# Kernel tuning notes

Hardware: AMD Instinct MI355X
Metric: run time of the kernel (lower is better)

## Reference

```python
import jax, jax.numpy as jnp
import numpy as np

EPS = 1e-8

def rms_norm(x, scale):
    # full RMSNorm over last dim (p < 0 branch): norm/sqrt(d)
    d = x.shape[-1]
    norm = jnp.linalg.norm(x, ord=2, axis=-1, keepdims=True)
    rms = norm * (d ** -0.5)
    return scale * (x / (rms + EPS))

def setup_inputs() -> dict:
    key = jax.random.key(0)
    ks = jax.random.split(key, 4)
    B, N, C, H = 2, 2048, 1024, 16
    hd = C // H
    x = jax.random.normal(ks[0], (B, N, C), dtype=jnp.float32)
    Wqkv = jax.random.normal(ks[1], (C, 3 * C), dtype=jnp.float32) * (C ** -0.5)
    Wproj = jax.random.normal(ks[2], (C, C), dtype=jnp.float32) * (C ** -0.5)
    bproj = jnp.zeros((C,), dtype=jnp.float32)
    q_scale = jnp.ones((hd,), dtype=jnp.float32)
    k_scale = jnp.ones((hd,), dtype=jnp.float32)
    return {"x": x, "Wqkv": Wqkv, "Wproj": Wproj, "bproj": bproj,
            "q_scale": q_scale, "k_scale": k_scale}

def reference(x, Wqkv, Wproj, bproj, q_scale, k_scale):
    B, N, C = x.shape
    H = 16
    hd = C // H
    scale = hd ** -0.5
    qkv = (x @ Wqkv).reshape(B, N, 3, H, hd)
    qkv = jnp.transpose(qkv, (2, 0, 3, 1, 4))  # t b h n c
    q, k, v = qkv[0], qkv[1], qkv[2]
    q = rms_norm(q, q_scale)
    k = rms_norm(k, k_scale)
    attn = jnp.einsum('bhnc,bhmc->bhnm', q, k) * scale
    attn = jax.nn.softmax(attn, axis=-1)
    out = jnp.einsum('bhnm,bhmc->bhnc', attn, v)
    out = jnp.transpose(out, (0, 2, 1, 3)).reshape(B, N, C)
    return out @ Wproj + bproj
```

## Files before the change

### kernel.cpp

```cpp
#include <hip/hip_runtime.h>


typedef _Float16 half_t;
typedef __attribute__((ext_vector_type(2))) __fp16 fp16x2;
typedef __attribute__((ext_vector_type(4))) _Float16 half4v;
typedef __attribute__((ext_vector_type(8))) _Float16 half8;
typedef __attribute__((ext_vector_type(4))) float f32x4;

#define DI __device__ __forceinline__

DI void gl_lds16(const void* g, void* l) {
    __builtin_amdgcn_global_load_lds((const __attribute__((address_space(1))) void*)g,
                                     (__attribute__((address_space(3))) void*)l, 16, 0, 0);
}

DI float exp2_fast(float x) {
    float r;
    asm("v_exp_f32 %0, %1" : "=v"(r) : "v"(x));
    return r;
}

__global__ void prep_all(const float* __restrict__ x, const float* __restrict__ Wqkv,
                         const float* __restrict__ Wproj, half_t* __restrict__ xh,
                         half_t* __restrict__ wqt, half_t* __restrict__ wpt) {
    __shared__ float t[32][33];
    int bid = blockIdx.x;
    if (bid < 4096) {
        int i = (bid * 256 + threadIdx.x) * 4;
        float4 v = *(const float4*)(x + i);
        half4v o;
        o[0] = (half_t)v.x; o[1] = (half_t)v.y; o[2] = (half_t)v.z; o[3] = (half_t)v.w;
        *(half4v*)(xh + i) = o;
    } else if (bid < 4096 + 3072) {
        int i = bid - 4096;
        int c0 = (i % 96) * 32, r0 = (i / 96) * 32;
        int tx = threadIdx.x & 31, ty = threadIdx.x >> 5;
#pragma unroll
        for (int k = 0; k < 4; k++)
            t[ty + 8 * k][tx] = Wqkv[(size_t)(r0 + ty + 8 * k) * 3072 + c0 + tx];
        __syncthreads();
#pragma unroll
        for (int k = 0; k < 4; k++)
            wqt[(size_t)(c0 + ty + 8 * k) * 1024 + r0 + tx] = (half_t)t[tx][ty + 8 * k];
    } else {
        int i = bid - 4096 - 3072;
        int c0 = (i % 32) * 32, r0 = (i / 32) * 32;
        int tx = threadIdx.x & 31, ty = threadIdx.x >> 5;
#pragma unroll
        for (int k = 0; k < 4; k++)
            t[ty + 8 * k][tx] = Wproj[(size_t)(r0 + ty + 8 * k) * 1024 + c0 + tx];
        __syncthreads();
#pragma unroll
        for (int k = 0; k < 4; k++)
            wpt[(size_t)(c0 + ty + 8 * k) * 1024 + r0 + tx] = (half_t)t[tx][ty + 8 * k];
    }
}

__global__ __launch_bounds__(256) void gemm_qkv(
    const half_t* __restrict__ A, const half_t* __restrict__ Bt,
    const float* __restrict__ qs, const float* __restrict__ ks,
    half_t* __restrict__ qh, half_t* __restrict__ kh, half_t* __restrict__ vth) {
    const int K = 1024;
    __shared__ __align__(16) half_t Al[2][128 * 64];
    __shared__ __align__(16) half_t Bl[2][128 * 64];
    int tid = threadIdx.x;
    int w = tid >> 6, l = tid & 63;
    int wr = w >> 1, wc = w & 1;
    int g = l >> 4, r = l & 15;
    int m0 = blockIdx.x * 128, n0 = blockIdx.y * 128;
    f32x4 acc[4][4] = {};

#define STAGE_QKV(kt, buf)                                                        \
    {                                                                             \
        _Pragma("unroll")                                                         \
        for (int p = 0; p < 4; p++) {                                             \
            int ci = p * 256 + tid;                                               \
            int row = ci >> 3, c = ci & 7, lc = c ^ (row & 7);                    \
            gl_lds16(A + (size_t)(m0 + row) * K + (kt) * 64 + lc * 8,             \
                     &Al[buf][0] + ci * 8);                                       \
            gl_lds16(Bt + (size_t)(n0 + row) * K + (kt) * 64 + lc * 8,            \
                     &Bl[buf][0] + ci * 8);                                       \
        }                                                                         \
    }

    STAGE_QKV(0, 0);
    __syncthreads();
    int cur = 0;
    for (int kt = 0; kt < 16; kt++) {
        if (kt < 15) STAGE_QKV(kt + 1, cur ^ 1);
#pragma unroll
        for (int ks2 = 0; ks2 < 2; ks2++) {
            half8 af[4], bf[4];
#pragma unroll
            for (int i = 0; i < 4; i++) {
                int row = wr * 64 + i * 16 + r;
                af[i] = *(const half8*)(&Al[cur][0] + row * 64 + (((4 * ks2 + g) ^ (row & 7)) << 3));
                int rowb = wc * 64 + i * 16 + r;
                bf[i] = *(const half8*)(&Bl[cur][0] + rowb * 64 + (((4 * ks2 + g) ^ (rowb & 7)) << 3));
            }
#pragma unroll
            for (int i = 0; i < 4; i++)
#pragma unroll
                for (int j = 0; j < 4; j++)
                    acc[i][j] = __builtin_amdgcn_mfma_f32_16x16x32_f16(af[i], bf[j], acc[i][j], 0, 0, 0);
        }
        __syncthreads();
        cur ^= 1;
    }

    int tsec = n0 >> 10;
    if (tsec == 2) {
#pragma unroll
        for (int i = 0; i < 4; i++)
#pragma unroll
            for (int j = 0; j < 4; j++) {
                int gcol = n0 + wc * 64 + j * 16 + r;
                int h = (gcol >> 6) & 15;
                int f = gcol & 63;
                int growb = m0 + wr * 64 + i * 16 + g * 4;
                int b = growb >> 11;
                int n = growb & 2047;
                half4v pv;
#pragma unroll
                for (int rr = 0; rr < 4; rr++) pv[rr] = (half_t)acc[i][j][rr];
                *(half4v*)(vth + ((size_t)(b * 16 + h) * 64 + f) * 2048 + n) = pv;
            }
    } else {
        const float* sc = (tsec == 0) ? qs : ks;
        half_t* dst = (tsec == 0) ? qh : kh;
        float extra = (tsec == 0) ? (0.125f * 1.44269504f) : 1.0f;
        float scv[4];
#pragma unroll
        for (int j = 0; j < 4; j++) scv[j] = sc[j * 16 + r];
#pragma unroll
        for (int i = 0; i < 4; i++)
#pragma unroll
            for (int rr = 0; rr < 4; rr++) {
                float ss = 0.f;
#pragma unroll
                for (int j = 0; j < 4; j++) ss += acc[i][j][rr] * acc[i][j][rr];
#pragma unroll
                for (int d = 1; d < 16; d <<= 1) ss += __shfl_xor(ss, d, 64);
                float inv = extra / (sqrtf(ss) * 0.125f + 1e-8f);
                int grow = m0 + wr * 64 + i * 16 + g * 4 + rr;
                int b = grow >> 11;
                int n = grow & 2047;
#pragma unroll
                for (int j = 0; j < 4; j++) {
                    int gcol = n0 + wc * 64 + j * 16 + r;
                    int h = (gcol >> 6) & 15;
                    int f = gcol & 63;
                    dst[((size_t)(b * 16 + h) * 2048 + n) * 64 + f] =
                        (half_t)(acc[i][j][rr] * inv * scv[j]);
                }
            }
    }
}

__global__ __launch_bounds__(512, 4) void attn(
    const half_t* __restrict__ qh, const half_t* __restrict__ kh,
    const half_t* __restrict__ vth, half_t* __restrict__ aoh) {
    int bh = blockIdx.y;
    int q0 = blockIdx.x * 128;
    const half_t* Qp = qh + (size_t)bh * 2048 * 64;
    const half_t* Kp = kh + (size_t)bh * 2048 * 64;
    const half_t* Vp = vth + (size_t)bh * 64 * 2048;
    __shared__ __align__(16) half_t Kl[2][64 * 64];
    __shared__ __align__(16) half_t Vl[2][64 * 64];
    __shared__ __align__(16) half_t Pl[8][16 * 64];
    int tid = threadIdx.x, w = tid >> 6, l = tid & 63, g = l >> 4, r = l & 15;

    int srow = tid >> 3, sc = tid & 7, slc = sc ^ (srow & 7);
    const half_t* kst = Kp + (size_t)srow * 64 + slc * 8;
    const half_t* vst = Vp + (size_t)srow * 2048 + slc * 8;

    int koff[8], voff[8], poffw[4], poffr[2];
#pragma unroll
    for (int ks = 0; ks < 2; ks++)
#pragma unroll
        for (int tt = 0; tt < 4; tt++) {
            int row = tt * 16 + r;
            koff[ks * 4 + tt] = row * 64 + (((4 * ks + g) ^ (row & 7)) << 3);
        }
#pragma unroll
    for (int ks2 = 0; ks2 < 2; ks2++)
#pragma unroll
        for (int cf = 0; cf < 4; cf++) {
            int row = cf * 16 + r;
            voff[ks2 * 4 + cf] = row * 64 + (((4 * ks2 + g) ^ (row & 7)) << 3);
        }
#pragma unroll
    for (int tt = 0; tt < 4; tt++)
        poffw[tt] = r * 64 + (((2 * tt + (g >> 1)) ^ (r & 7)) << 3) + (g & 1) * 4;
#pragma unroll
    for (int ks2 = 0; ks2 < 2; ks2++)
        poffr[ks2] = r * 64 + (((4 * ks2 + g) ^ (r & 7)) << 3);
    half_t* Pw = &Pl[w][0];

    half8 qf[2];
#pragma unroll
    for (int ks = 0; ks < 2; ks++)
        qf[ks] = *(const half8*)(Qp + (size_t)(q0 + w * 16 + r) * 64 + ks * 32 + g * 8);

    f32x4 o[4] = {};
    float m = -1e30f, lsum = 0.f;

    gl_lds16(kst, &Kl[0][0] + tid * 8);
    gl_lds16(vst, &Vl[0][0] + tid * 8);
    __syncthreads();

#define ATTN_TILE(BUF, T)                                                          \
    {                                                                              \
        if ((T) < 31) {                                                            \
            gl_lds16(kst + ((T) + 1) * 4096, &Kl[(BUF) ^ 1][0] + tid * 8);         \
            gl_lds16(vst + ((T) + 1) * 64, &Vl[(BUF) ^ 1][0] + tid * 8);           \
        }                                                                          \
        const half_t* Kc = &Kl[BUF][0];                                            \
        const half_t* Vc = &Vl[BUF][0];                                            \
        f32x4 s[4] = {};                                                           \
        _Pragma("unroll")                                                          \
        for (int ks = 0; ks < 2; ks++)                                             \
            _Pragma("unroll")                                                      \
            for (int tt = 0; tt < 4; tt++) {                                       \
                half8 kf = *(const half8*)(Kc + koff[ks * 4 + tt]);                \
                s[tt] = __builtin_amdgcn_mfma_f32_16x16x32_f16(kf, qf[ks], s[tt], 0, 0, 0); \
            }                                                                      \
        float mx = -1e30f;                                                         \
        _Pragma("unroll")                                                          \
        for (int tt = 0; tt < 4; tt++)                                             \
            mx = fmaxf(mx, fmaxf(fmaxf(s[tt][0], s[tt][1]), fmaxf(s[tt][2], s[tt][3]))); \
        mx = fmaxf(mx, __shfl_xor(mx, 16, 64));                                    \
        mx = fmaxf(mx, __shfl_xor(mx, 32, 64));                                    \
        if (!__all(mx <= m + 11.0f)) {                                             \
            float mn = fmaxf(m, mx);                                               \
            float fac = exp2_fast(m - mn);                                         \
            lsum *= fac;                                                           \
            _Pragma("unroll")                                                      \
            for (int cf = 0; cf < 4; cf++) {                                       \
                o[cf][0] *= fac; o[cf][1] *= fac; o[cf][2] *= fac; o[cf][3] *= fac; \
            }                                                                      \
            m = mn;                                                                \
        }                                                                          \
        _Pragma("unroll")                                                          \
        for (int tt = 0; tt < 4; tt++)                                             \
            _Pragma("unroll")                                                      \
            for (int e = 0; e < 4; e++) {                                          \
                float p = exp2_fast(s[tt][e] - m);                                 \
                s[tt][e] = p;                                                      \
                lsum += p;                                                         \
            }                                                                      \
        _Pragma("unroll")                                                          \
        for (int tt = 0; tt < 4; tt++) {                                           \
            fp16x2 a = __builtin_amdgcn_cvt_pkrtz(s[tt][0], s[tt][1]);             \
            fp16x2 b = __builtin_amdgcn_cvt_pkrtz(s[tt][2], s[tt][3]);             \
            half4v v4;                                                             \
            v4[0] = (half_t)a[0]; v4[1] = (half_t)a[1];                            \
            v4[2] = (half_t)b[0]; v4[3] = (half_t)b[1];                            \
            *(half4v*)(Pw + poffw[tt]) = v4;                                       \
        }                                                                          \
        _Pragma("unroll")                                                          \
        for (int ks2 = 0; ks2 < 2; ks2++) {                                        \
            half8 pf = *(const half8*)(Pw + poffr[ks2]);                           \
            _Pragma("unroll")                                                      \
            for (int cf = 0; cf < 4; cf++) {                                       \
                half8 vf = *(const half8*)(Vc + voff[ks2 * 4 + cf]);               \
                o[cf] = __builtin_amdgcn_mfma_f32_16x16x32_f16(vf, pf, o[cf], 0, 0, 0); \
            }                                                                      \
        }                                                                          \
        __syncthreads();                                                           \
    }

    for (int t = 0; t < 32; t += 2) {
        ATTN_TILE(0, t);
        ATTN_TILE(1, t + 1);
    }

    lsum += __shfl_xor(lsum, 16, 64);
    lsum += __shfl_xor(lsum, 32, 64);

    int b = bh >> 4, h = bh & 15;
    int n = q0 + w * 16 + r;
    float inv = 1.0f / lsum;
#pragma unroll
    for (int cf = 0; cf < 4; cf++) {
        half4v ov;
#pragma unroll
        for (int reg = 0; reg < 4; reg++) ov[reg] = (half_t)(o[cf][reg] * inv);
        *(half4v*)(aoh + ((size_t)b * 2048 + n) * 1024 + h * 64 + cf * 16 + g * 4) = ov;
    }
}

__global__ __launch_bounds__(256) void gemm_proj(
    const half_t* __restrict__ A, const half_t* __restrict__ Bt,
    const float* __restrict__ bias, float* __restrict__ out) {
    const int K = 1024;
    __shared__ __align__(16) half_t Al[128 * 64];
    __shared__ __align__(16) half_t Bl[128 * 64];
    int tid = threadIdx.x, w = tid >> 6, l = tid & 63;
    int wr = w >> 1, wc = w & 1, g = l >> 4, r = l & 15;
    int m0 = blockIdx.x * 128, n0 = blockIdx.y * 128;
    f32x4 acc[4][4] = {};

    for (int k0 = 0; k0 < K; k0 += 64) {
#pragma unroll
        for (int p = 0; p < 4; p++) {
            int ci = (p * 4 + w) * 64 + l;
            int row = ci >> 3, c = ci & 7;
            int lc = c ^ (row & 7);
            gl_lds16(A + (size_t)(m0 + row) * K + k0 + lc * 8, Al + (p * 4 + w) * 512);
            gl_lds16(Bt + (size_t)(n0 + row) * K + k0 + lc * 8, Bl + (p * 4 + w) * 512);
        }
        __syncthreads();
#pragma unroll
        for (int ks = 0; ks < 2; ks++) {
            half8 af[4], bf[4];
#pragma unroll
            for (int i = 0; i < 4; i++) {
                int row = wr * 64 + i * 16 + r;
                af[i] = *(const half8*)(Al + row * 64 + (((4 * ks + g) ^ (row & 7)) << 3));
                int rowb = wc * 64 + i * 16 + r;
                bf[i] = *(const half8*)(Bl + rowb * 64 + (((4 * ks + g) ^ (rowb & 7)) << 3));
            }
#pragma unroll
            for (int i = 0; i < 4; i++)
#pragma unroll
                for (int j = 0; j < 4; j++)
                    acc[i][j] = __builtin_amdgcn_mfma_f32_16x16x32_f16(af[i], bf[j], acc[i][j], 0, 0, 0);
        }
        __syncthreads();
    }

#pragma unroll
    for (int i = 0; i < 4; i++)
#pragma unroll
        for (int j = 0; j < 4; j++) {
            int gcol = n0 + wc * 64 + j * 16 + r;
            float bv = bias[gcol];
#pragma unroll
            for (int rr = 0; rr < 4; rr++) {
                int grow = m0 + wr * 64 + i * 16 + g * 4 + rr;
                out[(size_t)grow * 1024 + gcol] = acc[i][j][rr] + bv;
            }
        }
}

extern "C" void kernel_launch(void* const* d_in, const int* in_sizes, int n_in,
                              void* d_out, int out_size, void* d_ws, size_t ws_size,
                              hipStream_t stream) {
    const float* x = (const float*)d_in[0];
    const float* Wqkv = (const float*)d_in[1];
    const float* Wproj = (const float*)d_in[2];
    const float* bproj = (const float*)d_in[3];
    const float* qscale = (const float*)d_in[4];
    const float* kscale = (const float*)d_in[5];
    float* out = (float*)d_out;

    char* ws = (char*)d_ws;
    half_t* xh  = (half_t*)(ws + 0);
    half_t* wqt = (half_t*)(ws + 8388608);
    half_t* wpt = (half_t*)(ws + 14680064);
    half_t* qh  = (half_t*)(ws + 16777216);
    half_t* kh  = (half_t*)(ws + 25165824);
    half_t* vth = (half_t*)(ws + 33554432);
    half_t* aoh = (half_t*)(ws + 41943040);

    prep_all<<<8192, 256, 0, stream>>>(x, Wqkv, Wproj, xh, wqt, wpt);
    gemm_qkv<<<dim3(32, 24), 256, 0, stream>>>(xh, wqt, qscale, kscale, qh, kh, vth);
    attn<<<dim3(16, 32), 512, 0, stream>>>(qh, kh, vth, aoh);
    gemm_proj<<<dim3(32, 8), 256, 0, stream>>>(aoh, wpt, bproj, out);
}
```

Baseline: 131.4 us.

## Software-pipeline attention with triple-buffered K/V and overlapped QK and softmax-PV

Restructures the attention main loop so the QK^T MFMAs for the next key tile are issued before the softmax and PV of the current tile. K/V move from double to triple buffering in LDS, with a prologue and epilogue that keep the tile order intact. The aim is to hide softmax and exp latency behind matrix work and keep MFMA units busier. In exchange the kernel needs more LDS and more registers for the second score accumulator, which may lower the number of resident blocks per CU.

```diff
diff --git a/kernel.cpp b/kernel.cpp
--- a/kernel.cpp
+++ b/kernel.cpp
@@ -165,8 +165,8 @@
     const half_t* Qp = qh + (size_t)bh * 2048 * 64;
     const half_t* Kp = kh + (size_t)bh * 2048 * 64;
     const half_t* Vp = vth + (size_t)bh * 64 * 2048;
-    __shared__ __align__(16) half_t Kl[2][64 * 64];
-    __shared__ __align__(16) half_t Vl[2][64 * 64];
+    __shared__ __align__(16) half_t Kl[3][64 * 64];
+    __shared__ __align__(16) half_t Vl[3][64 * 64];
     __shared__ __align__(16) half_t Pl[8][16 * 64];
     int tid = threadIdx.x, w = tid >> 6, l = tid & 63, g = l >> 4, r = l & 15;
 
@@ -203,32 +203,35 @@
         qf[ks] = *(const half8*)(Qp + (size_t)(q0 + w * 16 + r) * 64 + ks * 32 + g * 8);
 
     f32x4 o[4] = {};
+    f32x4 sE[4], sO[4];
     float m = -1e30f, lsum = 0.f;
 
-    gl_lds16(kst, &Kl[0][0] + tid * 8);
-    gl_lds16(vst, &Vl[0][0] + tid * 8);
-    __syncthreads();
-
-#define ATTN_TILE(BUF, T)                                                          \
+#define STAGE_T(T, IDX)                                                            \
     {                                                                              \
-        if ((T) < 31) {                                                            \
-            gl_lds16(kst + ((T) + 1) * 4096, &Kl[(BUF) ^ 1][0] + tid * 8);         \
-            gl_lds16(vst + ((T) + 1) * 64, &Vl[(BUF) ^ 1][0] + tid * 8);           \
-        }                                                                          \
-        const half_t* Kc = &Kl[BUF][0];                                            \
-        const half_t* Vc = &Vl[BUF][0];                                            \
-        f32x4 s[4] = {};                                                           \
+        gl_lds16(kst + (T) * 4096, &Kl[IDX][0] + tid * 8);                         \
+        gl_lds16(vst + (T) * 64, &Vl[IDX][0] + tid * 8);                           \
+    }
+
+#define QK_STEP(KB, S)                                                             \
+    {                                                                              \
+        const half_t* Kc = &Kl[KB][0];                                             \
+        _Pragma("unroll")                                                          \
+        for (int tt = 0; tt < 4; tt++) S[tt] = (f32x4){0.f, 0.f, 0.f, 0.f};        \
         _Pragma("unroll")                                                          \
         for (int ks = 0; ks < 2; ks++)                                             \
             _Pragma("unroll")                                                      \
             for (int tt = 0; tt < 4; tt++) {                                       \
                 half8 kf = *(const half8*)(Kc + koff[ks * 4 + tt]);                \
-                s[tt] = __builtin_amdgcn_mfma_f32_16x16x32_f16(kf, qf[ks], s[tt], 0, 0, 0); \
+                S[tt] = __builtin_amdgcn_mfma_f32_16x16x32_f16(kf, qf[ks], S[tt], 0, 0, 0); \
             }                                                                      \
+    }
+
+#define SM_PV(S, VB)                                                               \
+    {                                                                              \
         float mx = -1e30f;                                                         \
         _Pragma("unroll")                                                          \
         for (int tt = 0; tt < 4; tt++)                                             \
-            mx = fmaxf(mx, fmaxf(fmaxf(s[tt][0], s[tt][1]), fmaxf(s[tt][2], s[tt][3]))); \
+            mx = fmaxf(mx, fmaxf(fmaxf(S[tt][0], S[tt][1]), fmaxf(S[tt][2], S[tt][3]))); \
         mx = fmaxf(mx, __shfl_xor(mx, 16, 64));                                    \
         mx = fmaxf(mx, __shfl_xor(mx, 32, 64));                                    \
         if (!__all(mx <= m + 11.0f)) {                                             \
@@ -245,19 +248,20 @@
         for (int tt = 0; tt < 4; tt++)                                             \
             _Pragma("unroll")                                                      \
             for (int e = 0; e < 4; e++) {                                          \
-                float p = exp2_fast(s[tt][e] - m);                                 \
-                s[tt][e] = p;                                                      \
+                float p = exp2_fast(S[tt][e] - m);                                 \
+                S[tt][e] = p;                                                      \
                 lsum += p;                                                         \
             }                                                                      \
         _Pragma("unroll")                                                          \
         for (int tt = 0; tt < 4; tt++) {                                           \
-            fp16x2 a = __builtin_amdgcn_cvt_pkrtz(s[tt][0], s[tt][1]);             \
-            fp16x2 b = __builtin_amdgcn_cvt_pkrtz(s[tt][2], s[tt][3]);             \
+            fp16x2 a = __builtin_amdgcn_cvt_pkrtz(S[tt][0], S[tt][1]);             \
+            fp16x2 b = __builtin_amdgcn_cvt_pkrtz(S[tt][2], S[tt][3]);             \
             half4v v4;                                                             \
             v4[0] = (half_t)a[0]; v4[1] = (half_t)a[1];                            \
             v4[2] = (half_t)b[0]; v4[3] = (half_t)b[1];                            \
             *(half4v*)(Pw + poffw[tt]) = v4;                                       \
         }                                                                          \
+        const half_t* Vc = &Vl[VB][0];                                             \
         _Pragma("unroll")                                                          \
         for (int ks2 = 0; ks2 < 2; ks2++) {                                        \
             half8 pf = *(const half8*)(Pw + poffr[ks2]);                           \
@@ -267,13 +271,26 @@
                 o[cf] = __builtin_amdgcn_mfma_f32_16x16x32_f16(vf, pf, o[cf], 0, 0, 0); \
             }                                                                      \
         }                                                                          \
-        __syncthreads();                                                           \
-    }
-
-    for (int t = 0; t < 32; t += 2) {
-        ATTN_TILE(0, t);
-        ATTN_TILE(1, t + 1);
-    }
+    }
+
+    STAGE_T(0, 0);
+    __syncthreads();
+    QK_STEP(0, sE);
+    STAGE_T(1, 1);
+    __syncthreads();
+
+    for (int k = 0; k < 5; k++) {
+        QK_STEP(1, sO); STAGE_T(6 * k + 2, 2); SM_PV(sE, 0); __syncthreads();
+        QK_STEP(2, sE); STAGE_T(6 * k + 3, 0); SM_PV(sO, 1); __syncthreads();
+        QK_STEP(0, sO); STAGE_T(6 * k + 4, 1); SM_PV(sE, 2); __syncthreads();
+        QK_STEP(1, sE); STAGE_T(6 * k + 5, 2); SM_PV(sO, 0); __syncthreads();
+        QK_STEP(2, sO); STAGE_T(6 * k + 6, 0); SM_PV(sE, 1); __syncthreads();
+        QK_STEP(0, sE); STAGE_T(6 * k + 7, 1); SM_PV(sO, 2); __syncthreads();
+    }
+
+    QK_STEP(1, sO);
+    SM_PV(sE, 0);
+    SM_PV(sO, 1);
 
     lsum += __shfl_xor(lsum, 16, 64);
     lsum += __shfl_xor(lsum, 32, 64);
```

After: 130.8 us. No clear change (-0.5%).

## Replace LDS P round-trip with permlane swaps and cheaper max-check in attention

Applied to the files above, without the earlier changes.

The attention kernel no longer writes softmax probabilities to shared memory and reads them back in B-operand layout. It rearranges the packed fp16 P values across lanes in registers with v_permlane32_swap and v_permlane16_swap. The lazy-rescale check now compares each score against a threshold and computes the row max with shuffles only when rescaling is needed. Launch bounds raise the occupancy hint from 4 to 6 waves, which cuts LDS use but may force register spills.

```diff
diff --git a/kernel.cpp b/kernel.cpp
--- a/kernel.cpp
+++ b/kernel.cpp
@@ -6,6 +6,7 @@
 typedef __attribute__((ext_vector_type(4))) _Float16 half4v;
 typedef __attribute__((ext_vector_type(8))) _Float16 half8;
 typedef __attribute__((ext_vector_type(4))) float f32x4;
+typedef __attribute__((ext_vector_type(4))) unsigned uint4v;
 
 #define DI __device__ __forceinline__
 
@@ -18,6 +19,18 @@
     float r;
     asm("v_exp_f32 %0, %1" : "=v"(r) : "v"(x));
     return r;
+}
+
+DI void pl32_swap(unsigned& a, unsigned& b) {
+    asm("v_permlane32_swap_b32 %0, %1" : "+v"(a), "+v"(b));
+}
+DI void pl16_swap(unsigned& a, unsigned& b) {
+    asm("v_permlane16_swap_b32 %0, %1" : "+v"(a), "+v"(b));
+}
+
+DI unsigned pk_u32(float lo, float hi) {
+    fp16x2 t = __builtin_amdgcn_cvt_pkrtz(lo, hi);
+    return *(unsigned*)&t;
 }
 
 __global__ void prep_all(const float* __restrict__ x, const float* __restrict__ Wqkv,
@@ -157,7 +170,7 @@
     }
 }
 
-__global__ __launch_bounds__(512, 4) void attn(
+__global__ __launch_bounds__(512, 6) void attn(
     const half_t* __restrict__ qh, const half_t* __restrict__ kh,
     const half_t* __restrict__ vth, half_t* __restrict__ aoh) {
     int bh = blockIdx.y;
@@ -167,14 +180,13 @@
     const half_t* Vp = vth + (size_t)bh * 64 * 2048;
     __shared__ __align__(16) half_t Kl[2][64 * 64];
     __shared__ __align__(16) half_t Vl[2][64 * 64];
-    __shared__ __align__(16) half_t Pl[8][16 * 64];
     int tid = threadIdx.x, w = tid >> 6, l = tid & 63, g = l >> 4, r = l & 15;
 
     int srow = tid >> 3, sc = tid & 7, slc = sc ^ (srow & 7);
     const half_t* kst = Kp + (size_t)srow * 64 + slc * 8;
     const half_t* vst = Vp + (size_t)srow * 2048 + slc * 8;
 
-    int koff[8], voff[8], poffw[4], poffr[2];
+    int koff[8], voff[8];
 #pragma unroll
     for (int ks = 0; ks < 2; ks++)
 #pragma unroll
@@ -189,13 +201,6 @@
             int row = cf * 16 + r;
             voff[ks2 * 4 + cf] = row * 64 + (((4 * ks2 + g) ^ (row & 7)) << 3);
         }
-#pragma unroll
-    for (int tt = 0; tt < 4; tt++)
-        poffw[tt] = r * 64 + (((2 * tt + (g >> 1)) ^ (r & 7)) << 3) + (g & 1) * 4;
-#pragma unroll
-    for (int ks2 = 0; ks2 < 2; ks2++)
-        poffr[ks2] = r * 64 + (((4 * ks2 + g) ^ (r & 7)) << 3);
-    half_t* Pw = &Pl[w][0];
 
     half8 qf[2];
 #pragma unroll
@@ -225,13 +230,19 @@
                 half8 kf = *(const half8*)(Kc + koff[ks * 4 + tt]);                \
                 s[tt] = __builtin_amdgcn_mfma_f32_16x16x32_f16(kf, qf[ks], s[tt], 0, 0, 0); \
             }                                                                      \
-        float mx = -1e30f;                                                         \
+        float thr = m + 11.0f;                                                     \
+        bool ok = true;                                                            \
         _Pragma("unroll")                                                          \
         for (int tt = 0; tt < 4; tt++)                                             \
-            mx = fmaxf(mx, fmaxf(fmaxf(s[tt][0], s[tt][1]), fmaxf(s[tt][2], s[tt][3]))); \
-        mx = fmaxf(mx, __shfl_xor(mx, 16, 64));                                    \
-        mx = fmaxf(mx, __shfl_xor(mx, 32, 64));                                    \
-        if (!__all(mx <= m + 11.0f)) {                                             \
+            _Pragma("unroll")                                                      \
+            for (int e = 0; e < 4; e++) ok = ok && (s[tt][e] <= thr);              \
+        if (!__all(ok)) {                                                          \
+            float mx = -1e30f;                                                     \
+            _Pragma("unroll")                                                      \
+            for (int tt = 0; tt < 4; tt++)                                         \
+                mx = fmaxf(mx, fmaxf(fmaxf(s[tt][0], s[tt][1]), fmaxf(s[tt][2], s[tt][3]))); \
+            mx = fmaxf(mx, __shfl_xor(mx, 16, 64));                                \
+            mx = fmaxf(mx, __shfl_xor(mx, 32, 64));                                \
             float mn = fmaxf(m, mx);                                               \
             float fac = exp2_fast(m - mn);                                         \
             lsum *= fac;                                                           \
@@ -249,18 +260,20 @@
                 s[tt][e] = p;                                                      \
                 lsum += p;                                                         \
             }                                                                      \
+        unsigned W[4][2];                                                          \
         _Pragma("unroll")                                                          \
         for (int tt = 0; tt < 4; tt++) {                                           \
-            fp16x2 a = __builtin_amdgcn_cvt_pkrtz(s[tt][0], s[tt][1]);             \
-            fp16x2 b = __builtin_amdgcn_cvt_pkrtz(s[tt][2], s[tt][3]);             \
-            half4v v4;                                                             \
-            v4[0] = (half_t)a[0]; v4[1] = (half_t)a[1];                            \
-            v4[2] = (half_t)b[0]; v4[3] = (half_t)b[1];                            \
-            *(half4v*)(Pw + poffw[tt]) = v4;                                       \
+            W[tt][0] = pk_u32(s[tt][0], s[tt][1]);                                 \
+            W[tt][1] = pk_u32(s[tt][2], s[tt][3]);                                 \
         }                                                                          \
         _Pragma("unroll")                                                          \
         for (int ks2 = 0; ks2 < 2; ks2++) {                                        \
-            half8 pf = *(const half8*)(Pw + poffr[ks2]);                           \
+            unsigned b0 = W[2 * ks2][0], b2 = W[2 * ks2 + 1][0];                   \
+            unsigned b1 = W[2 * ks2][1], b3 = W[2 * ks2 + 1][1];                   \
+            pl32_swap(b0, b2); pl16_swap(b0, b2);                                  \
+            pl32_swap(b1, b3); pl16_swap(b1, b3);                                  \
+            uint4v pw; pw[0] = b0; pw[1] = b1; pw[2] = b2; pw[3] = b3;             \
+            half8 pf = *(half8*)&pw;                                               \
             _Pragma("unroll")                                                      \
             for (int cf = 0; cf < 4; cf++) {                                       \
                 half8 vf = *(const half8*)(Vc + voff[ks2 * 4 + cf]);               \
```

After: 131.6 us. Within noise of the previous version (+0.2%).
